# Kernel tuning notes

Hardware: AMD Instinct MI355X
Metric: run time of the kernel (lower is better)

## Reference

```python
import jax, jax.numpy as jnp
import numpy as np

B, V, D = 1024, 50000, 300
EPS = 1e-7


def setup_inputs() -> dict:
    key = jax.random.key(0)
    k1, k2 = jax.random.split(key)
    # soft multi-hot label mask over the vocab (torch code multiplies floats)
    labels = jax.random.uniform(k1, (B, V), dtype=jnp.float32)
    # pretrained word2vec-style embedding table
    weight = jax.random.normal(k2, (V, D), dtype=jnp.float32)
    return {"labels": labels, "weight": weight}


def reference(labels, weight):
    # torch: mul(weight, labels[:, :, None]).sum(1)  ==  labels @ weight
    attr = jnp.einsum('bv,vd->bd', labels, weight)  # (B, D)
    # L2 normalize: attr / (sqrt(sum(attr^2, 1)) + 1e-7)
    norm = jnp.sqrt(jnp.sum(attr * attr, axis=1, keepdims=True))
    return attr / (norm + EPS)
```

## Files before the change

### kernel.cpp

```cpp
#include <hip/hip_runtime.h>
#include <hip/hip_bf16.h>
#include <math.h>

typedef __bf16 bf16;
typedef bf16 bf16x8 __attribute__((ext_vector_type(8)));
typedef float f32x4 __attribute__((ext_vector_type(4)));

constexpr int Mdim = 1024;
constexpr int Kdim = 50000;
constexpr int Kpad = 50048;
constexpr int Ndim = 300;
constexpr int NP   = 320;

constexpr int BM = 64, BN = 320, BK = 64;
constexpr int MT = Mdim / BM;
constexpr int ROWB = BK * 2;

__device__ __forceinline__ bf16x8 bzero8() {
    bf16x8 v;
#pragma unroll
    for (int e = 0; e < 8; ++e) v[e] = (bf16)0.0f;
    return v;
}

__device__ __forceinline__ bf16* swz(bf16* base, int row, int colByte) {
    return (bf16*)((char*)base + row * ROWB + (colByte ^ ((row & 7) << 4)));
}
__device__ __forceinline__ const bf16* swz(const bf16* base, int row, int colByte) {
    return (const bf16*)((const char*)base + row * ROWB + (colByte ^ ((row & 7) << 4)));
}

__device__ __forceinline__ void dma16(const void* g, void* l) {
    __builtin_amdgcn_global_load_lds(
        (const __attribute__((address_space(1))) unsigned int*)g,
        (__attribute__((address_space(3))) unsigned int*)l, 16, 0, 0);
}

constexpr int TK = 64;
constexpr int TS = 301;
__global__ __launch_bounds__(256) void transpose_w(const float* __restrict__ W,
                                                   bf16* __restrict__ Wt)
{
    __shared__ bf16 tile[TK * TS];
    const int k0 = blockIdx.x * TK;
    const int t  = threadIdx.x;

    for (int c = t; c < 64 * 75; c += 256) {
        const int kk = c / 75;
        const int ch = c % 75;
        const int k  = k0 + kk;
        float4 v = make_float4(0.f, 0.f, 0.f, 0.f);
        if (k < Kdim) v = *(const float4*)(W + (size_t)k * Ndim + ch * 4);
        bf16* p = &tile[kk * TS + ch * 4];
        p[0] = (bf16)v.x; p[1] = (bf16)v.y; p[2] = (bf16)v.z; p[3] = (bf16)v.w;
    }
    __syncthreads();
    for (int c = t; c < NP * 8; c += 256) {
        const int n  = c >> 3;
        const int ch = c & 7;
        const int k  = k0 + ch * 8;
        bf16x8 v = bzero8();
        if (n < Ndim) {
#pragma unroll
            for (int j = 0; j < 8; ++j)
                v[j] = tile[(ch * 8 + j) * TS + n];
        }
        *(bf16x8*)(Wt + (size_t)n * Kpad + k) = v;
    }
}

template<int SPLIT, int SEGLEN, bool ATOMIC>
__global__ __launch_bounds__(512, 4) void gemm_kernel(const float* __restrict__ A,
                                                      const bf16* __restrict__ Wt,
                                                      float* __restrict__ out)
{
    __shared__ bf16 As[BM * BK];
    __shared__ bf16 Bs[BN * BK];

    const int bx   = blockIdx.x;
    const int mt   = bx & (MT - 1);
    const int ks   = bx >> 4;
    const int m0   = mt * BM;
    const int kbeg = ks * SEGLEN;
    const int kend = min(kbeg + SEGLEN, Kdim);

    const int t    = threadIdx.x;
    const int lane = t & 63;
    const int wave = t >> 6;
    const int wm   = wave >> 2;
    const int wn   = wave & 3;
    const int lm   = lane & 15;
    const int lq   = lane >> 4;

    const int arow = t >> 3;
    const int acol = (t & 7) * 8;
    const float* aptr = A + (size_t)(m0 + arow) * Kdim;
    float4 af[2];

    auto loadA = [&](int k0) {
        const int k = k0 + acol;
        if (k + 8 <= kend) {
            af[0] = *(const float4*)(aptr + k);
            af[1] = *(const float4*)(aptr + k + 4);
        } else {
            af[0] = make_float4(0.f, 0.f, 0.f, 0.f);
            af[1] = make_float4(0.f, 0.f, 0.f, 0.f);
        }
    };
    auto storeA = [&]() {
        bf16x8 v;
        v[0]=(bf16)af[0].x; v[1]=(bf16)af[0].y; v[2]=(bf16)af[0].z; v[3]=(bf16)af[0].w;
        v[4]=(bf16)af[1].x; v[5]=(bf16)af[1].y; v[6]=(bf16)af[1].z; v[7]=(bf16)af[1].w;
        *(bf16x8*)swz(As, arow, acol * 2) = v;
    };

    const int r8   = lane >> 3;
    const int cswz = ((lane & 7) ^ r8) * 16;
    auto stageB = [&](int k0) {
#pragma unroll
        for (int i = 0; i < 5; ++i) {
            const int chunk = wave * 5 + i;
            const int row   = chunk * 8 + r8;
            const char* g = (const char*)Wt + ((size_t)row * Kpad + k0) * 2 + cswz;
            dma16(g, (char*)Bs + chunk * 1024);
        }
    };

    f32x4 acc[2][5] = {};

    loadA(kbeg);
    for (int k0 = kbeg; k0 < kend; k0 += BK) {
        __syncthreads();
        stageB(k0);
        storeA();
        if (k0 + BK < kend) loadA(k0 + BK);
        __syncthreads();
#pragma unroll
        for (int s = 0; s < 2; ++s) {
            bf16x8 a[2], b[5];
#pragma unroll
            for (int i = 0; i < 2; ++i)
                a[i] = *(const bf16x8*)swz(As, wm * 32 + i * 16 + lm, s * 64 + lq * 16);
#pragma unroll
            for (int j = 0; j < 5; ++j)
                b[j] = *(const bf16x8*)swz(Bs, wn * 80 + j * 16 + lm, s * 64 + lq * 16);
#pragma unroll
            for (int i = 0; i < 2; ++i)
#pragma unroll
                for (int j = 0; j < 5; ++j)
                    acc[i][j] = __builtin_amdgcn_mfma_f32_16x16x32_bf16(a[i], b[j], acc[i][j], 0, 0, 0);
        }
    }

    const int col0 = wn * 80 + lm;
    const int rloc = wm * 32 + lq * 4;
    if (ATOMIC) {
#pragma unroll
        for (int i = 0; i < 2; ++i)
#pragma unroll
            for (int j = 0; j < 5; ++j)
#pragma unroll
                for (int r = 0; r < 4; ++r)
                    atomicAdd(&out[(size_t)(m0 + rloc + i * 16 + r) * NP + col0 + j * 16],
                              acc[i][j][r]);
    } else {
        float* P = out + (size_t)ks * Mdim * NP;
#pragma unroll
        for (int i = 0; i < 2; ++i)
#pragma unroll
            for (int j = 0; j < 5; ++j)
#pragma unroll
                for (int r = 0; r < 4; ++r)
                    P[(size_t)(m0 + rloc + i * 16 + r) * NP + col0 + j * 16] = acc[i][j][r];
    }
}

__global__ __launch_bounds__(320) void reduce_norm_k(const float* __restrict__ P,
                                                     float* __restrict__ out,
                                                     int split)
{
    const int b = blockIdx.x;
    const int t = threadIdx.x;
    float v = 0.f;
    for (int ks = 0; ks < split; ++ks)
        v += P[((size_t)ks * Mdim + b) * NP + t];
    float ss = v * v;
#pragma unroll
    for (int o = 32; o > 0; o >>= 1) ss += __shfl_down(ss, o, 64);
    __shared__ float wsum[5];
    __shared__ float scale;
    if ((t & 63) == 0) wsum[t >> 6] = ss;
    __syncthreads();
    if (t == 0) {
        float s = wsum[0] + wsum[1] + wsum[2] + wsum[3] + wsum[4];
        scale = 1.0f / (sqrtf(s) + 1e-7f);
    }
    __syncthreads();
    if (t < Ndim) out[(size_t)b * Ndim + t] = v * scale;
}

__global__ __launch_bounds__(320) void normalize_k(const float* __restrict__ Cacc,
                                                   float* __restrict__ out)
{
    const int b = blockIdx.x;
    const int t = threadIdx.x;
    float v = 0.f;
    if (t < Ndim) v = Cacc[(size_t)b * NP + t];
    float ss = v * v;
#pragma unroll
    for (int o = 32; o > 0; o >>= 1) ss += __shfl_down(ss, o, 64);
    __shared__ float wsum[5];
    __shared__ float scale;
    if ((t & 63) == 0) wsum[t >> 6] = ss;
    __syncthreads();
    if (t == 0) {
        float s = wsum[0] + wsum[1] + wsum[2] + wsum[3] + wsum[4];
        scale = 1.0f / (sqrtf(s) + 1e-7f);
    }
    __syncthreads();
    if (t < Ndim) out[(size_t)b * Ndim + t] = v * scale;
}

extern "C" void kernel_launch(void* const* d_in, const int* in_sizes, int n_in,
                              void* d_out, int out_size, void* d_ws, size_t ws_size,
                              hipStream_t stream)
{
    const float* labels = (const float*)d_in[0];
    const float* weight = (const float*)d_in[1];
    float* out = (float*)d_out;

    bf16* Wt = (bf16*)d_ws;
    const size_t wtBytes  = (size_t)NP * Kpad * sizeof(bf16);
    float* aux = (float*)((char*)d_ws + wtBytes);
    const size_t perSplit = (size_t)Mdim * NP * sizeof(float);

    transpose_w<<<dim3(Kpad / TK), dim3(256), 0, stream>>>(weight, Wt);

    if (ws_size >= wtBytes + 49 * perSplit) {
        gemm_kernel<49, 1024, false><<<dim3(MT * 49), dim3(512), 0, stream>>>(labels, Wt, aux);
        reduce_norm_k<<<dim3(Mdim), dim3(320), 0, stream>>>(aux, out, 49);
    } else if (ws_size >= wtBytes + 16 * perSplit) {
        gemm_kernel<16, 3136, false><<<dim3(MT * 16), dim3(512), 0, stream>>>(labels, Wt, aux);
        reduce_norm_k<<<dim3(Mdim), dim3(320), 0, stream>>>(aux, out, 16);
    } else {
        hipMemsetAsync(aux, 0, perSplit, stream);
        gemm_kernel<49, 1024, true><<<dim3(MT * 49), dim3(512), 0, stream>>>(labels, Wt, aux);
        normalize_k<<<dim3(Mdim), dim3(320), 0, stream>>>(aux, out);
    }
}
```

Measured before the change: 378.1 us.

## Double-buffer LDS tiles with software pipelining and XCD-aware block remap

The GEMM's A and B tiles are double-buffered in shared memory, so the next tile's global-to-LDS DMA and A loads are issued before the current tile's MFMAs. Explicit waitcnt plus a single barrier per iteration replace the two __syncthreads. Blocks are remapped so consecutive K-splits land on the same XCD, and the split changes from 49×1024 to 48×1088. A-load bounds checks are replaced by a clamped pointer, relying on Wt's zero padding to cancel out-of-segment reads. Doubling LDS to about 96KB per block cuts resident blocks per CU, which trades occupancy for overlap.

```diff
diff --git a/kernel.cpp b/kernel.cpp
--- a/kernel.cpp
+++ b/kernel.cpp
@@ -70,16 +70,24 @@
 }
 
 template<int SPLIT, int SEGLEN, bool ATOMIC>
-__global__ __launch_bounds__(512, 4) void gemm_kernel(const float* __restrict__ A,
+__global__ __launch_bounds__(512, 2) void gemm_kernel(const float* __restrict__ A,
                                                       const bf16* __restrict__ Wt,
                                                       float* __restrict__ out)
 {
-    __shared__ bf16 As[BM * BK];
-    __shared__ bf16 Bs[BN * BK];
-
-    const int bx   = blockIdx.x;
-    const int mt   = bx & (MT - 1);
-    const int ks   = bx >> 4;
+    __shared__ bf16 As[2][BM * BK];
+    __shared__ bf16 Bs[2][BN * BK];
+
+    const int bx = blockIdx.x;
+    int mt, ks;
+    if (SPLIT == 48) {
+        const int x = bx & 7;
+        const int i = bx >> 3;
+        ks = x * 6 + (i >> 4);
+        mt = i & 15;
+    } else {
+        mt = bx & (MT - 1);
+        ks = bx >> 4;
+    }
     const int m0   = mt * BM;
     const int kbeg = ks * SEGLEN;
     const int kend = min(kbeg + SEGLEN, Kdim);
@@ -94,62 +102,84 @@
 
     const int arow = t >> 3;
     const int acol = (t & 7) * 8;
-    const float* aptr = A + (size_t)(m0 + arow) * Kdim;
+    const size_t alim  = (size_t)Mdim * Kdim - 8;
+    const size_t abase = (size_t)(m0 + arow) * Kdim + acol;
     float4 af[2];
 
     auto loadA = [&](int k0) {
-        const int k = k0 + acol;
-        if (k + 8 <= kend) {
-            af[0] = *(const float4*)(aptr + k);
-            af[1] = *(const float4*)(aptr + k + 4);
-        } else {
-            af[0] = make_float4(0.f, 0.f, 0.f, 0.f);
-            af[1] = make_float4(0.f, 0.f, 0.f, 0.f);
-        }
-    };
-    auto storeA = [&]() {
+        size_t off = abase + (size_t)k0;
+        if (off > alim) off = alim;
+        const float* p = A + off;
+        af[0] = *(const float4*)p;
+        af[1] = *(const float4*)(p + 4);
+    };
+    auto storeA = [&](int buf) {
         bf16x8 v;
         v[0]=(bf16)af[0].x; v[1]=(bf16)af[0].y; v[2]=(bf16)af[0].z; v[3]=(bf16)af[0].w;
         v[4]=(bf16)af[1].x; v[5]=(bf16)af[1].y; v[6]=(bf16)af[1].z; v[7]=(bf16)af[1].w;
-        *(bf16x8*)swz(As, arow, acol * 2) = v;
+        *(bf16x8*)swz(As[buf], arow, acol * 2) = v;
     };
 
     const int r8   = lane >> 3;
     const int cswz = ((lane & 7) ^ r8) * 16;
-    auto stageB = [&](int k0) {
+    auto stageB = [&](int k0, int buf) {
 #pragma unroll
         for (int i = 0; i < 5; ++i) {
             const int chunk = wave * 5 + i;
             const int row   = chunk * 8 + r8;
             const char* g = (const char*)Wt + ((size_t)row * Kpad + k0) * 2 + cswz;
-            dma16(g, (char*)Bs + chunk * 1024);
+            dma16(g, (char*)Bs[buf] + chunk * 1024);
         }
     };
 
     f32x4 acc[2][5] = {};
 
-    loadA(kbeg);
-    for (int k0 = kbeg; k0 < kend; k0 += BK) {
-        __syncthreads();
-        stageB(k0);
-        storeA();
-        if (k0 + BK < kend) loadA(k0 + BK);
-        __syncthreads();
+    auto compute = [&](int buf) {
 #pragma unroll
         for (int s = 0; s < 2; ++s) {
             bf16x8 a[2], b[5];
 #pragma unroll
             for (int i = 0; i < 2; ++i)
-                a[i] = *(const bf16x8*)swz(As, wm * 32 + i * 16 + lm, s * 64 + lq * 16);
+                a[i] = *(const bf16x8*)swz(As[buf], wm * 32 + i * 16 + lm, s * 64 + lq * 16);
 #pragma unroll
             for (int j = 0; j < 5; ++j)
-                b[j] = *(const bf16x8*)swz(Bs, wn * 80 + j * 16 + lm, s * 64 + lq * 16);
+                b[j] = *(const bf16x8*)swz(Bs[buf], wn * 80 + j * 16 + lm, s * 64 + lq * 16);
 #pragma unroll
             for (int i = 0; i < 2; ++i)
 #pragma unroll
                 for (int j = 0; j < 5; ++j)
                     acc[i][j] = __builtin_amdgcn_mfma_f32_16x16x32_bf16(a[i], b[j], acc[i][j], 0, 0, 0);
         }
+    };
+
+    if (kbeg < kend) {
+        loadA(kbeg);
+        stageB(kbeg, 0);
+        storeA(0);
+        loadA(kbeg + BK);
+        __builtin_amdgcn_sched_barrier(0);
+        asm volatile("s_waitcnt vmcnt(2) lgkmcnt(0)" ::: "memory");
+        __builtin_amdgcn_s_barrier();
+        __builtin_amdgcn_sched_barrier(0);
+
+        int cur = 0;
+        int k0  = kbeg;
+        for (; k0 + BK < kend; k0 += BK) {
+            const int nb = cur ^ 1;
+            stageB(k0 + BK, nb);
+            __builtin_amdgcn_sched_barrier(0);
+            storeA(nb);
+            const bool more2 = (k0 + 2 * BK < kend);
+            if (more2) loadA(k0 + 2 * BK);
+            compute(cur);
+            __builtin_amdgcn_sched_barrier(0);
+            if (more2) asm volatile("s_waitcnt vmcnt(2) lgkmcnt(0)" ::: "memory");
+            else       asm volatile("s_waitcnt vmcnt(0) lgkmcnt(0)" ::: "memory");
+            __builtin_amdgcn_s_barrier();
+            __builtin_amdgcn_sched_barrier(0);
+            cur = nb;
+        }
+        compute(cur);
     }
 
     const int col0 = wn * 80 + lm;
@@ -236,15 +266,15 @@
 
     transpose_w<<<dim3(Kpad / TK), dim3(256), 0, stream>>>(weight, Wt);
 
-    if (ws_size >= wtBytes + 49 * perSplit) {
-        gemm_kernel<49, 1024, false><<<dim3(MT * 49), dim3(512), 0, stream>>>(labels, Wt, aux);
-        reduce_norm_k<<<dim3(Mdim), dim3(320), 0, stream>>>(aux, out, 49);
+    if (ws_size >= wtBytes + 48 * perSplit) {
+        gemm_kernel<48, 1088, false><<<dim3(MT * 48), dim3(512), 0, stream>>>(labels, Wt, aux);
+        reduce_norm_k<<<dim3(Mdim), dim3(320), 0, stream>>>(aux, out, 48);
     } else if (ws_size >= wtBytes + 16 * perSplit) {
-        gemm_kernel<16, 3136, false><<<dim3(MT * 16), dim3(512), 0, stream>>>(labels, Wt, aux);
+        gemm_kernel<16, 3200, false><<<dim3(MT * 16), dim3(512), 0, stream>>>(labels, Wt, aux);
         reduce_norm_k<<<dim3(Mdim), dim3(320), 0, stream>>>(aux, out, 16);
     } else {
         hipMemsetAsync(aux, 0, perSplit, stream);
-        gemm_kernel<49, 1024, true><<<dim3(MT * 49), dim3(512), 0, stream>>>(labels, Wt, aux);
+        gemm_kernel<48, 1088, true><<<dim3(MT * 48), dim3(512), 0, stream>>>(labels, Wt, aux);
         normalize_k<<<dim3(Mdim), dim3(320), 0, stream>>>(aux, out);
     }
 }
```

After: 371.8 us. No clear change (-1.7%).
